# Performance work log

Measured on AMD Instinct MI355X. Metric: run time of the kernel, lower is better.

Reference implementation:

```python
import jax, jax.numpy as jnp
import numpy as np
import math

DMODEL = 1024
N_EXPERTS = 32
EXPERT_SIZE = 512
N_HEADS = 4
TOKENS = 4096


def setup_inputs() -> dict:
    key = jax.random.key(0)
    k1, k2, k3, k4 = jax.random.split(key, 4)
    x = jax.random.normal(k1, (TOKENS, DMODEL), dtype=jnp.float32)
    keys_w = jax.random.normal(k2, (N_EXPERTS, DMODEL, EXPERT_SIZE), dtype=jnp.float32) * (DMODEL ** -0.5)
    values_w = jax.random.normal(k3, (N_EXPERTS, EXPERT_SIZE, DMODEL), dtype=jnp.float32) * ((N_EXPERTS * EXPERT_SIZE) ** -0.5)
    es = jax.random.normal(k4, (N_EXPERTS, DMODEL), dtype=jnp.float32) * (DMODEL ** -0.5)
    # renorm_keep_std(expert_sel, dim=1): row-normalize, then rescale to original global std
    std0 = jnp.std(es)
    es_n = es / jnp.linalg.norm(es, axis=1, keepdims=True)
    expert_sel = es_n * (std0 / jnp.std(es_n))
    return {"x": x, "keys": keys_w, "values": values_w, "expert_sel": expert_sel, "n_heads": N_HEADS}


def reference(x, keys, values, expert_sel, n_heads):
    # x: [T, d]; keys: [E, d, h]; values: [E, h, d]; expert_sel: [E, d]
    T, d = x.shape
    E = keys.shape[0]

    # routing logits
    sel_raw = x @ expert_sel.T  # [T, E]

    # entropy regularizer: mean (in log space) over tokens of log-softmax, then negative entropy
    logp = jax.nn.log_softmax(sel_raw, axis=-1)                 # [T, E]
    lm = jax.scipy.special.logsumexp(logp, axis=0) - math.log(T)  # [E]
    reg_loss = jnp.sum(lm * jnp.exp(lm))                        # -entropy_l(lm)

    # sigmoid selection + top-k experts per token
    sel = jax.nn.sigmoid(sel_raw)
    sel_val, sel_idx = jax.lax.top_k(sel, n_heads)              # [T, H]

    # expert up-projection (grouped GEMM): compute dense then gather selected experts
    scores_all = jnp.einsum('td,edh->teh', x, keys)             # [T, E, h]
    scores = jnp.take_along_axis(scores_all, sel_idx[:, :, None], axis=1)  # [T, H, h]
    scores = jax.nn.relu(scores) * sel_val[..., None]

    # combine: scatter weighted scores back to expert slots, then down-project
    onehot = jax.nn.one_hot(sel_idx, E, dtype=x.dtype)          # [T, H, E]
    dispatched = jnp.einsum('the,ths->tes', onehot, scores)     # [T, E, h]
    out = jnp.einsum('tes,esd->td', dispatched, values)         # [T, d]
    return out, reg_loss
```

## Files before the change

kernel.cpp:

```cpp
#include <hip/hip_runtime.h>
#include <hip/hip_bf16.h>

typedef unsigned short u16;
typedef unsigned int u32;
typedef __attribute__((ext_vector_type(4))) float f32x4;
typedef __attribute__((ext_vector_type(8))) short bf16x8;

#define TOKENS 4096
#define DMODEL 1024
#define NEXP 32
#define ESIZE 512

__device__ __forceinline__ u16 f2b(float f) {
  union { float f; u32 u; } v; v.f = f;
  u32 u = v.u;
  return (u16)((u + 0x7fffu + ((u >> 16) & 1u)) >> 16);
}

__device__ __forceinline__ u32 pk2(float a, float b) {
  union { __hip_bfloat162 h; u32 u; } v;
  v.h = __float22bfloat162_rn(make_float2(a, b));
  return v.u;
}

__device__ __forceinline__ float blo(u32 w) { union { u32 u; float f; } v; v.u = w << 16; return v.f; }
__device__ __forceinline__ float bhi(u32 w) { union { u32 u; float f; } v; v.u = w & 0xffff0000u; return v.f; }

typedef __attribute__((address_space(1))) const void as1_void;
typedef __attribute__((address_space(3))) void as3_void;
__device__ __forceinline__ void gl16(const void* g, void* l) {
  __builtin_amdgcn_global_load_lds((as1_void*)g, (as3_void*)l, 16, 0, 0);
}

__device__ __forceinline__ int swz(int row, int kk) {
  return row * 72 + ((((kk >> 3) ^ (row >> 2)) & 7) << 3) + (kk & 7);
}

__global__ __launch_bounds__(256) void k_esT(const float* __restrict__ es,
                                             float* __restrict__ esT4)
{
  int tid = threadIdx.x;
  int dblk = (blockIdx.x << 3) + (tid >> 5);
  int e = tid & 31;
  float4 v = *(const float4*)(es + (size_t)e * DMODEL + (dblk << 2));
  *((float4*)esT4 + (size_t)dblk * 32 + e) = v;
}

__device__ __forceinline__ void tr_tile(const float* __restrict__ src,
                                        u16* __restrict__ dst, int R, int C,
                                        int cx, int cy, int e, int t, float* smemf)
{
  float (*tile)[68] = (float(*)[68])smemf;
  int r0 = cy << 6, c0 = cx << 6;
  int rr = t >> 2, cb = (t & 3) << 4;
  const float* sp = src + ((size_t)e * R + r0 + rr) * C + c0 + cb;
#pragma unroll
  for (int j = 0; j < 4; ++j)
    *(float4*)&tile[rr][cb + (j << 2)] = *(const float4*)(sp + (j << 2));
  __syncthreads();
  int wr = t >> 2, wb = (t & 3) << 4;
  u32 q[8];
#pragma unroll
  for (int j = 0; j < 8; ++j)
    q[j] = pk2(tile[wb + (j << 1)][wr], tile[wb + (j << 1) + 1][wr]);
  u16* dp = dst + ((size_t)e * C + c0 + wr) * R + r0 + wb;
  *(uint4*)dp = make_uint4(q[0], q[1], q[2], q[3]);
  *(uint4*)(dp + 8) = make_uint4(q[4], q[5], q[6], q[7]);
}

__global__ __launch_bounds__(256) void k_mega1(
    const float* __restrict__ x, const float* __restrict__ esT4,
    float* __restrict__ selval, u32* __restrict__ selpk,
    float* __restrict__ blockpart, u16* __restrict__ xb,
    const float* __restrict__ keys, const float* __restrict__ values,
    u16* __restrict__ kb, u16* __restrict__ vb)
{
  __shared__ __align__(16) float smem[4352];
  int bid = blockIdx.x;
  int tid = threadIdx.x;

  if (bid >= 512 + 4096) {
    int i = bid - (512 + 4096);
    tr_tile(values, vb, ESIZE, DMODEL, i & 15, (i >> 4) & 7, i >> 7, tid, smem);
    return;
  }
  if (bid >= 512) {
    int i = bid - 512;
    tr_tile(keys, kb, DMODEL, ESIZE, i & 7, (i >> 3) & 15, i >> 7, tid, smem);
    return;
  }

  float (*part)[8][32] = (float(*)[8][32])smem;
  float (*ps)[32] = (float(*)[32])(smem + 1024);
  int w = tid >> 6, lane = tid & 63;
  int e = lane & 31, h = lane >> 5;
  int t0 = bid << 3;

  const float4* ev = (const float4*)esT4 + (size_t)((w << 6) + (h << 5)) * 32 + e;
  const float4* xv = (const float4*)x + ((size_t)t0 << 8) + (w << 6) + (h << 5);

  float acc[8];
#pragma unroll
  for (int tk = 0; tk < 8; ++tk) acc[tk] = 0.f;

#pragma unroll 2
  for (int i = 0; i < 32; ++i) {
    float4 b = ev[(size_t)i * 32];
#pragma unroll
    for (int tk = 0; tk < 8; ++tk) {
      float4 a = xv[(tk << 8) + i];
      acc[tk] += a.x * b.x + a.y * b.y + a.z * b.z + a.w * b.w;
    }
  }
#pragma unroll
  for (int tk = 0; tk < 8; ++tk) {
    float s = acc[tk] + __shfl_xor(acc[tk], 32);
    if (h == 0) part[w][tk][e] = s;
  }
  __syncthreads();

  int tk = tid >> 5, ge = tid & 31;
  {
    float r = part[0][tk][ge] + part[1][tk][ge] + part[2][tk][ge] + part[3][tk][ge];
    int t = t0 + tk;

    float m = r;
#pragma unroll
    for (int mk = 16; mk; mk >>= 1) m = fmaxf(m, __shfl_xor(m, mk));
    float sx = __expf(r - m);
#pragma unroll
    for (int mk = 16; mk; mk >>= 1) sx += __shfl_xor(sx, mk);
    ps[tk][ge] = __expf(r - (m + __logf(sx)));

    u32 packed = 0;
    float v = r;
#pragma unroll
    for (int it = 0; it < 4; ++it) {
      float bv = v; int bi = ge;
#pragma unroll
      for (int mk = 16; mk; mk >>= 1) {
        float ov = __shfl_xor(bv, mk); int oi = __shfl_xor(bi, mk);
        if (ov > bv || (ov == bv && oi < bi)) { bv = ov; bi = oi; }
      }
      packed |= (u32)bi << (8 * it);
      if (ge == it) selval[t * 4 + it] = 1.f / (1.f + __expf(-bv));
      if (ge == bi) v = -3.0e38f;
    }
    if (ge == 0) selpk[t] = packed;
  }
  __syncthreads();
  if (tid < 32) {
    float s = 0.f;
#pragma unroll
    for (int j = 0; j < 8; ++j) s += ps[j][tid];
    blockpart[bid * 32 + tid] = s;
  }

  if (xb) {
    const float4* src = (const float4*)x + ((size_t)bid << 11);
    u16* dst = xb + ((size_t)bid << 13);
#pragma unroll
    for (int j = 0; j < 8; ++j) {
      int idx = (j << 8) + tid;
      float4 a = src[idx];
      *(uint2*)(dst + (idx << 2)) = make_uint2(pk2(a.x, a.y), pk2(a.z, a.w));
    }
  }
}

__global__ __launch_bounds__(1024) void k_count(
    const u32* __restrict__ selpk, int* __restrict__ cnt, int* __restrict__ bucket)
{
  __shared__ int cl[32];
  int tid = threadIdx.x;
  if (tid < 32) cl[tid] = 0;
  __syncthreads();
  int ex[16], pos[16];
#pragma unroll
  for (int j = 0; j < 4; ++j) {
    int t = tid + (j << 10);
    u32 pk = selpk[t];
#pragma unroll
    for (int h = 0; h < 4; ++h) {
      int e = (pk >> (8 * h)) & 0xff;
      ex[j * 4 + h] = e;
      pos[j * 4 + h] = atomicAdd(&cl[e], 1);
    }
  }
#pragma unroll
  for (int j = 0; j < 4; ++j) {
    int t = tid + (j << 10);
#pragma unroll
    for (int h = 0; h < 4; ++h)
      bucket[ex[j * 4 + h] * TOKENS + pos[j * 4 + h]] = (t << 2) | h;
  }
  __syncthreads();
  if (tid < 32) cnt[tid] = cl[tid];
}

__global__ __launch_bounds__(256) void k_fin(const float* __restrict__ blockpart,
                                             float* __restrict__ out_reg)
{
  __shared__ float part[8][32];
  int tid = threadIdx.x;
  int e = tid & 31, c = tid >> 5;
  float s = 0.f;
  for (int b = c; b < 512; b += 8) s += blockpart[b * 32 + e];
  part[c][e] = s;
  __syncthreads();
  if (tid < 32) {
    float S = 0.f;
#pragma unroll
    for (int i = 0; i < 8; ++i) S += part[i][tid];
    float Pm = S * (1.0f / TOKENS);
    float rp = __logf(Pm) * Pm;
#pragma unroll
    for (int mk = 16; mk; mk >>= 1) rp += __shfl_xor(rp, mk);
    if (tid == 0) *out_reg = rp;
  }
}

#define GEMM_MACROS                                                                          \
  int wm = (w >> 1) << 6, wn = (w & 1) << 6;                                                 \
  int w32 = w << 5;                                                                          \
  int lg16 = (((l & 7) ^ (l >> 3)) << 4);

#define STAGE(BUF, K0) do {                                                                  \
  _Pragma("unroll") for (int i_ = 0; i_ < 4; ++i_)                                           \
    gl16(gA[i_] + ((K0) << 1), (void*)&Ab[BUF][(((w << 2) + i_) << 9)]);                     \
  _Pragma("unroll") for (int i_ = 0; i_ < 4; ++i_)                                           \
    gl16(gB[i_] + ((K0) << 1), (void*)&Bb[BUF][(((w << 2) + i_) << 9)]);                     \
} while (0)

#define COMPUTE(CUR) do {                                                                    \
  _Pragma("unroll") for (int kh_ = 0; kh_ < 2; ++kh_) {                                      \
    bf16x8 af_[4], bf_[4];                                                                   \
    int gg_ = (kh_ << 2) + (l >> 4);                                                         \
    _Pragma("unroll") for (int mi_ = 0; mi_ < 4; ++mi_) {                                    \
      int row_ = wm + (mi_ << 4) + (l & 15);                                                 \
      af_[mi_] = *(const bf16x8*)&Ab[CUR][(row_ << 6) + ((gg_ ^ (row_ & 7)) << 3)];          \
    }                                                                                        \
    _Pragma("unroll") for (int ni_ = 0; ni_ < 4; ++ni_) {                                    \
      int row_ = wn + (ni_ << 4) + (l & 15);                                                 \
      bf_[ni_] = *(const bf16x8*)&Bb[CUR][(row_ << 6) + ((gg_ ^ (row_ & 7)) << 3)];          \
    }                                                                                        \
    _Pragma("unroll") for (int mi_ = 0; mi_ < 4; ++mi_)                                      \
      _Pragma("unroll") for (int ni_ = 0; ni_ < 4; ++ni_)                                    \
        acc[mi_][ni_] = __builtin_amdgcn_mfma_f32_16x16x32_bf16(af_[mi_], bf_[ni_],          \
                                                                acc[mi_][ni_], 0, 0, 0);     \
  }                                                                                          \
} while (0)

#define KLOOP(NT) do {                                                                       \
  STAGE(0, 0);                                                                               \
  STAGE(1, 64);                                                                              \
  _Pragma("unroll 1")                                                                        \
  for (int t_ = 0; t_ < (NT); ++t_) {                                                        \
    int cur_ = t_ & 1;                                                                       \
    if (t_ + 1 < (NT)) { asm volatile("s_waitcnt vmcnt(8)" ::: "memory"); }                  \
    else               { asm volatile("s_waitcnt vmcnt(0)" ::: "memory"); }                  \
    asm volatile("s_barrier" ::: "memory");                                                  \
    COMPUTE(cur_);                                                                           \
    asm volatile("s_barrier" ::: "memory");                                                  \
    if (t_ + 2 < (NT)) STAGE(cur_, (t_ + 2) << 6);                                           \
  }                                                                                          \
} while (0)

#define XCD_DECODE(SUB_NS_BITS)                                                              \
  int bid = blockIdx.x;                                                                      \
  int q_ = bid >> 3, sub_ = q_ & 15;                                                         \
  int e = ((q_ >> 4) << 3) | (bid & 7);                                                      \
  int ns = sub_ & ((1 << (SUB_NS_BITS)) - 1);                                                \
  int mz = sub_ >> (SUB_NS_BITS);

__global__ __launch_bounds__(256, 2) void k_up(
    const u16* __restrict__ xb, const u16* __restrict__ kb,
    const float* __restrict__ selval, const int* __restrict__ cnt,
    const int* __restrict__ bucket, const u16* __restrict__ zeros,
    u16* __restrict__ scores)
{
  XCD_DECODE(2);
  int ne = cnt[e];
  if ((mz << 7) >= ne) return;
  int nb0 = ns << 7;
  int tid = threadIdx.x, l = tid & 63, w = tid >> 6;

  __shared__ __align__(16) u16 Ab[2][8192];
  __shared__ __align__(16) u16 Bb[2][8192];
  __shared__ int slot_l[128];
  __shared__ float gate_l[128];

  GEMM_MACROS;

  const char* gB[4];
#pragma unroll
  for (int i = 0; i < 4; ++i) {
    int n = nb0 + w32 + (i << 3) + (l >> 3);
    gB[i] = (const char*)(kb + ((size_t)e * ESIZE + n) * DMODEL) + lg16;
  }

  for (int mt = mz; (mt << 7) < ne; mt += 4) {
    int row0 = mt << 7;
    int rem = ne - row0; if (rem > 128) rem = 128;
    __syncthreads();
    if (tid < 128) {
      int slot = -1; float g = 0.f;
      if (tid < rem) { slot = bucket[e * TOKENS + row0 + tid]; g = selval[slot]; }
      slot_l[tid] = slot; gate_l[tid] = g;
    }
    __syncthreads();

    const char* gA[4];
#pragma unroll
    for (int i = 0; i < 4; ++i) {
      int s = slot_l[w32 + (i << 3) + (l >> 3)];
      gA[i] = ((s >= 0) ? (const char*)(xb + (size_t)(s >> 2) * DMODEL)
                        : (const char*)zeros) + lg16;
    }

    f32x4 acc[4][4];
#pragma unroll
    for (int i = 0; i < 4; ++i)
#pragma unroll
      for (int j = 0; j < 4; ++j) acc[i][j] = (f32x4){0.f, 0.f, 0.f, 0.f};

    KLOOP(16);

#pragma unroll
    for (int mi = 0; mi < 4; ++mi) {
      int rbase = wm + (mi << 4) + ((l >> 4) << 2);
#pragma unroll
      for (int rr = 0; rr < 4; ++rr) {
        int r = rbase + rr;
        if (r < rem) {
          float g = gate_l[r];
          u16* so = scores + (size_t)slot_l[r] * ESIZE + nb0 + wn + (l & 15);
#pragma unroll
          for (int ni = 0; ni < 4; ++ni)
            so[ni << 4] = f2b(fmaxf(acc[mi][ni][rr], 0.f) * g);
        }
      }
    }
  }
}

__global__ __launch_bounds__(256, 2) void k_down(
    const u16* __restrict__ scores, const u16* __restrict__ vb,
    const int* __restrict__ cnt, const int* __restrict__ bucket,
    const u16* __restrict__ zeros, u16* __restrict__ stage)
{
  XCD_DECODE(3);
  int ne = cnt[e];
  if ((mz << 7) >= ne) return;
  int nb0 = ns << 7;
  int tid = threadIdx.x, l = tid & 63, w = tid >> 6;

  __shared__ __align__(16) u16 Ab[2][8192];
  __shared__ __align__(16) u16 Bb[2][8192];
  __shared__ int slot_l[128];

  GEMM_MACROS;

  const char* gB[4];
#pragma unroll
  for (int i = 0; i < 4; ++i) {
    int n = nb0 + w32 + (i << 3) + (l >> 3);
    gB[i] = (const char*)(vb + ((size_t)e * DMODEL + n) * ESIZE) + lg16;
  }

  for (int mt = mz; (mt << 7) < ne; mt += 2) {
    int row0 = mt << 7;
    int rem = ne - row0; if (rem > 128) rem = 128;
    __syncthreads();
    if (tid < 128) {
      int slot = -1;
      if (tid < rem) slot = bucket[e * TOKENS + row0 + tid];
      slot_l[tid] = slot;
    }
    __syncthreads();

    const char* gA[4];
#pragma unroll
    for (int i = 0; i < 4; ++i) {
      int s = slot_l[w32 + (i << 3) + (l >> 3)];
      gA[i] = ((s >= 0) ? (const char*)(scores + (size_t)s * ESIZE)
                        : (const char*)zeros) + lg16;
    }

    f32x4 acc[4][4];
#pragma unroll
    for (int i = 0; i < 4; ++i)
#pragma unroll
      for (int j = 0; j < 4; ++j) acc[i][j] = (f32x4){0.f, 0.f, 0.f, 0.f};

    KLOOP(8);

#pragma unroll
    for (int mi = 0; mi < 4; ++mi) {
      int rbase = wm + (mi << 4) + ((l >> 4) << 2);
#pragma unroll
      for (int rr = 0; rr < 4; ++rr) {
        int r = rbase + rr;
        if (r < rem) {
          u16* so = stage + (size_t)slot_l[r] * DMODEL + nb0 + wn + (l & 15);
#pragma unroll
          for (int ni = 0; ni < 4; ++ni)
            so[ni << 4] = f2b(acc[mi][ni][rr]);
        }
      }
    }
  }
}

__global__ __launch_bounds__(256) void k_final(const u16* __restrict__ stage,
                                               float* __restrict__ out)
{
  int tid = threadIdx.x;
  int t = (blockIdx.x << 1) + (tid >> 7);
  int d0 = (tid & 127) << 3;
  const u16* r0 = stage + ((size_t)t << 12) + d0;
  uint4 a0 = *(const uint4*)(r0);
  uint4 a1 = *(const uint4*)(r0 + 1024);
  uint4 a2 = *(const uint4*)(r0 + 2048);
  uint4 a3 = *(const uint4*)(r0 + 3072);
  float4 lo4, hi4;
  lo4.x = blo(a0.x) + blo(a1.x) + blo(a2.x) + blo(a3.x);
  lo4.y = bhi(a0.x) + bhi(a1.x) + bhi(a2.x) + bhi(a3.x);
  lo4.z = blo(a0.y) + blo(a1.y) + blo(a2.y) + blo(a3.y);
  lo4.w = bhi(a0.y) + bhi(a1.y) + bhi(a2.y) + bhi(a3.y);
  hi4.x = blo(a0.z) + blo(a1.z) + blo(a2.z) + blo(a3.z);
  hi4.y = bhi(a0.z) + bhi(a1.z) + bhi(a2.z) + bhi(a3.z);
  hi4.z = blo(a0.w) + blo(a1.w) + blo(a2.w) + blo(a3.w);
  hi4.w = bhi(a0.w) + bhi(a1.w) + bhi(a2.w) + bhi(a3.w);
  float* o = out + (size_t)t * DMODEL + d0;
  *(float4*)o = lo4;
  *(float4*)(o + 4) = hi4;
}

__global__ __launch_bounds__(256, 2) void k_up_rs(
    const float* __restrict__ x, const float* __restrict__ keys,
    const float* __restrict__ selval, const int* __restrict__ cnt,
    const int* __restrict__ bucket, u16* __restrict__ scores)
{
  int bid = blockIdx.x;
  int pair = bid & 127, mz = bid >> 7;
  int e = pair >> 2, ns = pair & 3;
  int ne = cnt[e];
  if ((mz << 7) >= ne) return;
  int nb0 = ns << 7;
  int tid = threadIdx.x;

  __shared__ __align__(16) u16 Abuf[2][128 * 72];
  __shared__ __align__(16) u16 Bbuf[2][128 * 72];
  __shared__ int slot_l[128];
  __shared__ float gate_l[128];

  const float* Kb = keys + (size_t)e * (DMODEL * ESIZE) + nb0;
  int arow = tid >> 1, ac0 = (tid & 1) << 5;
  int bn = tid & 31, bk0 = (tid >> 5) << 3;
  int lane = tid & 63, w = tid >> 6;
  int wm = (w >> 1) << 6, wn = (w & 1) << 6;

  for (int mt = mz; (mt << 7) < ne; mt += 4) {
    int row0 = mt << 7;
    int rem = ne - row0; if (rem > 128) rem = 128;
    __syncthreads();
    if (tid < 128) {
      int slot = -1; float g = 0.f;
      if (tid < rem) { slot = bucket[e * TOKENS + row0 + tid]; g = selval[slot]; }
      slot_l[tid] = slot; gate_l[tid] = g;
    }
    __syncthreads();

    int aslot = slot_l[arow];
    const float* xr = (aslot >= 0) ? (x + (size_t)(aslot >> 2) * DMODEL + ac0) : nullptr;
    const float* bp = Kb + (size_t)bk0 * ESIZE + (bn << 2);

    f32x4 acc[4][4];
#pragma unroll
    for (int i = 0; i < 4; ++i)
#pragma unroll
      for (int j = 0; j < 4; ++j) acc[i][j] = (f32x4){0.f, 0.f, 0.f, 0.f};

    float4 ar[8], br[8];
#define LOADA_UP(K) do { if (xr) { const float4* p_ = (const float4*)(xr + (K)); \
    _Pragma("unroll") for (int i_ = 0; i_ < 8; ++i_) ar[i_] = p_[i_]; } \
    else { _Pragma("unroll") for (int i_ = 0; i_ < 8; ++i_) ar[i_] = make_float4(0.f,0.f,0.f,0.f); } } while (0)
#define LOADB_RS(K, LDB) do { const float* q_ = bp + (size_t)(K) * (LDB); \
    _Pragma("unroll") for (int r_ = 0; r_ < 8; ++r_) br[r_] = *(const float4*)(q_ + (size_t)r_ * (LDB)); } while (0)
#define CVTWR_A(NB) do { _Pragma("unroll") for (int g_ = 0; g_ < 4; ++g_) { \
    u32 q0_ = pk2(ar[2*g_].x, ar[2*g_].y),   q1_ = pk2(ar[2*g_].z, ar[2*g_].w); \
    u32 q2_ = pk2(ar[2*g_+1].x, ar[2*g_+1].y), q3_ = pk2(ar[2*g_+1].z, ar[2*g_+1].w); \
    *(uint4*)&Abuf[NB][swz(arow, ac0 + 8*g_)] = make_uint4(q0_,q1_,q2_,q3_); } } while (0)
#define CVTWR_B(NB) do { \
    { u32 q0_=pk2(br[0].x,br[1].x),q1_=pk2(br[2].x,br[3].x),q2_=pk2(br[4].x,br[5].x),q3_=pk2(br[6].x,br[7].x); \
      *(uint4*)&Bbuf[NB][swz((bn<<2)+0, bk0)] = make_uint4(q0_,q1_,q2_,q3_); } \
    { u32 q0_=pk2(br[0].y,br[1].y),q1_=pk2(br[2].y,br[3].y),q2_=pk2(br[4].y,br[5].y),q3_=pk2(br[6].y,br[7].y); \
      *(uint4*)&Bbuf[NB][swz((bn<<2)+1, bk0)] = make_uint4(q0_,q1_,q2_,q3_); } \
    { u32 q0_=pk2(br[0].z,br[1].z),q1_=pk2(br[2].z,br[3].z),q2_=pk2(br[4].z,br[5].z),q3_=pk2(br[6].z,br[7].z); \
      *(uint4*)&Bbuf[NB][swz((bn<<2)+2, bk0)] = make_uint4(q0_,q1_,q2_,q3_); } \
    { u32 q0_=pk2(br[0].w,br[1].w),q1_=pk2(br[2].w,br[3].w),q2_=pk2(br[4].w,br[5].w),q3_=pk2(br[6].w,br[7].w); \
      *(uint4*)&Bbuf[NB][swz((bn<<2)+3, bk0)] = make_uint4(q0_,q1_,q2_,q3_); } } while (0)
#define MFMA_RS(CUR) do { _Pragma("unroll") for (int kh_ = 0; kh_ < 2; ++kh_) { \
    int kk_ = (kh_ << 5) | ((lane >> 4) << 3); \
    bf16x8 af_[4], bf_[4]; \
    _Pragma("unroll") for (int mi_ = 0; mi_ < 4; ++mi_) \
      af_[mi_] = *(const bf16x8*)&Abuf[CUR][swz(wm + (mi_ << 4) + (lane & 15), kk_)]; \
    _Pragma("unroll") for (int ni_ = 0; ni_ < 4; ++ni_) \
      bf_[ni_] = *(const bf16x8*)&Bbuf[CUR][swz(wn + (ni_ << 4) + (lane & 15), kk_)]; \
    _Pragma("unroll") for (int mi_ = 0; mi_ < 4; ++mi_) \
      _Pragma("unroll") for (int ni_ = 0; ni_ < 4; ++ni_) \
        acc[mi_][ni_] = __builtin_amdgcn_mfma_f32_16x16x32_bf16(af_[mi_], bf_[ni_], acc[mi_][ni_], 0, 0, 0); \
  } } while (0)

    LOADA_UP(0); LOADB_RS(0, ESIZE);
    CVTWR_A(0); CVTWR_B(0);
    __syncthreads();
    int cur = 0;
    for (int k0 = 0; k0 < DMODEL; k0 += 64) {
      bool late = (k0 + 64 >= DMODEL);
      if (!late) { LOADA_UP(k0 + 64); LOADB_RS(k0 + 64, ESIZE); }
      MFMA_RS(cur);
      if (!late) { CVTWR_A(cur ^ 1); CVTWR_B(cur ^ 1); }
      __syncthreads();
      cur ^= 1;
    }

#pragma unroll
    for (int mi = 0; mi < 4; ++mi) {
      int rbase = wm + (mi << 4) + ((lane >> 4) << 2);
#pragma unroll
      for (int rr = 0; rr < 4; ++rr) {
        int r = rbase + rr;
        if (r < rem) {
          float g = gate_l[r];
          u16* so = scores + (size_t)slot_l[r] * ESIZE + nb0 + wn + (lane & 15);
#pragma unroll
          for (int ni = 0; ni < 4; ++ni)
            so[ni << 4] = f2b(fmaxf(acc[mi][ni][rr], 0.f) * g);
        }
      }
    }
#undef LOADA_UP
#undef LOADB_RS
#undef CVTWR_A
#undef CVTWR_B
#undef MFMA_RS
  }
}

__global__ __launch_bounds__(256, 2) void k_down_rs(
    const u16* __restrict__ scores, const float* __restrict__ values,
    const int* __restrict__ cnt, const int* __restrict__ bucket,
    u16* __restrict__ stage, float* __restrict__ out)
{
  int bid = blockIdx.x;
  int pair = bid & 255, mz = bid >> 8;
  int e = pair >> 3, ns = pair & 7;
  int ne = cnt[e];
  if ((mz << 7) >= ne) return;
  int nb0 = ns << 7;
  int tid = threadIdx.x;

  __shared__ __align__(16) u16 Abuf[2][128 * 72];
  __shared__ __align__(16) u16 Bbuf[2][128 * 72];
  __shared__ int slot_l[128];

  const float* Vb = values + (size_t)e * (ESIZE * DMODEL) + nb0;
  int arow = tid >> 1, ac0 = (tid & 1) << 5;
  int bn = tid & 31, bk0 = (tid >> 5) << 3;
  int lane = tid & 63, w = tid >> 6;
  int wm = (w >> 1) << 6, wn = (w & 1) << 6;

  for (int mt = mz; (mt << 7) < ne; mt += 2) {
    int row0 = mt << 7;
    int rem = ne - row0; if (rem > 128) rem = 128;
    __syncthreads();
    if (tid < 128) {
      int slot = -1;
      if (tid < rem) slot = bucket[e * TOKENS + row0 + tid];
      slot_l[tid] = slot;
    }
    __syncthreads();

    int aslot = slot_l[arow];
    const u16* sr = (aslot >= 0) ? (scores + (size_t)aslot * ESIZE + ac0) : nullptr;
    const float* bp = Vb + (size_t)bk0 * DMODEL + (bn << 2);

    f32x4 acc[4][4];
#pragma unroll
    for (int i = 0; i < 4; ++i)
#pragma unroll
      for (int j = 0; j < 4; ++j) acc[i][j] = (f32x4){0.f, 0.f, 0.f, 0.f};

    uint4 a4[4]; float4 br[8];
#define LOADA_DN(K) do { if (sr) { const uint4* p_ = (const uint4*)(sr + (K)); \
    _Pragma("unroll") for (int i_ = 0; i_ < 4; ++i_) a4[i_] = p_[i_]; } \
    else { _Pragma("unroll") for (int i_ = 0; i_ < 4; ++i_) a4[i_] = make_uint4(0,0,0,0); } } while (0)
#define LOADB_RS(K, LDB) do { const float* q_ = bp + (size_t)(K) * (LDB); \
    _Pragma("unroll") for (int r_ = 0; r_ < 8; ++r_) br[r_] = *(const float4*)(q_ + (size_t)r_ * (LDB)); } while (0)
#define WR_A(NB) do { _Pragma("unroll") for (int g_ = 0; g_ < 4; ++g_) \
    *(uint4*)&Abuf[NB][swz(arow, ac0 + 8*g_)] = a4[g_]; } while (0)
#define CVTWR_B(NB) do { \
    { u32 q0_=pk2(br[0].x,br[1].x),q1_=pk2(br[2].x,br[3].x),q2_=pk2(br[4].x,br[5].x),q3_=pk2(br[6].x,br[7].x); \
      *(uint4*)&Bbuf[NB][swz((bn<<2)+0, bk0)] = make_uint4(q0_,q1_,q2_,q3_); } \
    { u32 q0_=pk2(br[0].y,br[1].y),q1_=pk2(br[2].y,br[3].y),q2_=pk2(br[4].y,br[5].y),q3_=pk2(br[6].y,br[7].y); \
      *(uint4*)&Bbuf[NB][swz((bn<<2)+1, bk0)] = make_uint4(q0_,q1_,q2_,q3_); } \
    { u32 q0_=pk2(br[0].z,br[1].z),q1_=pk2(br[2].z,br[3].z),q2_=pk2(br[4].z,br[5].z),q3_=pk2(br[6].z,br[7].z); \
      *(uint4*)&Bbuf[NB][swz((bn<<2)+2, bk0)] = make_uint4(q0_,q1_,q2_,q3_); } \
    { u32 q0_=pk2(br[0].w,br[1].w),q1_=pk2(br[2].w,br[3].w),q2_=pk2(br[4].w,br[5].w),q3_=pk2(br[6].w,br[7].w); \
      *(uint4*)&Bbuf[NB][swz((bn<<2)+3, bk0)] = make_uint4(q0_,q1_,q2_,q3_); } } while (0)
#define MFMA_RS(CUR) do { _Pragma("unroll") for (int kh_ = 0; kh_ < 2; ++kh_) { \
    int kk_ = (kh_ << 5) | ((lane >> 4) << 3); \
    bf16x8 af_[4], bf_[4]; \
    _Pragma("unroll") for (int mi_ = 0; mi_ < 4; ++mi_) \
      af_[mi_] = *(const bf16x8*)&Abuf[CUR][swz(wm + (mi_ << 4) + (lane & 15), kk_)]; \
    _Pragma("unroll") for (int ni_ = 0; ni_ < 4; ++ni_) \
      bf_[ni_] = *(const bf16x8*)&Bbuf[CUR][swz(wn + (ni_ << 4) + (lane & 15), kk_)]; \
    _Pragma("unroll") for (int mi_ = 0; mi_ < 4; ++mi_) \
      _Pragma("unroll") for (int ni_ = 0; ni_ < 4; ++ni_) \
        acc[mi_][ni_] = __builtin_amdgcn_mfma_f32_16x16x32_bf16(af_[mi_], bf_[ni_], acc[mi_][ni_], 0, 0, 0); \
  } } while (0)

    LOADA_DN(0); LOADB_RS(0, DMODEL);
    WR_A(0); CVTWR_B(0);
    __syncthreads();
    int cur = 0;
    for (int k0 = 0; k0 < ESIZE; k0 += 64) {
      bool late = (k0 + 64 >= ESIZE);
      if (!late) { LOADA_DN(k0 + 64); LOADB_RS(k0 + 64, DMODEL); }
      MFMA_RS(cur);
      if (!late) { WR_A(cur ^ 1); CVTWR_B(cur ^ 1); }
      __syncthreads();
      cur ^= 1;
    }

#pragma unroll
    for (int mi = 0; mi < 4; ++mi) {
      int rbase = wm + (mi << 4) + ((lane >> 4) << 2);
#pragma unroll
      for (int rr = 0; rr < 4; ++rr) {
        int r = rbase + rr;
        if (r < rem) {
          if (stage) {
            u16* so = stage + (size_t)slot_l[r] * DMODEL + nb0 + wn + (lane & 15);
#pragma unroll
            for (int ni = 0; ni < 4; ++ni)
              so[ni << 4] = f2b(acc[mi][ni][rr]);
          } else {
            int t = slot_l[r] >> 2;
            float* oo = out + (size_t)t * DMODEL + nb0 + wn + (lane & 15);
#pragma unroll
            for (int ni = 0; ni < 4; ++ni)
              atomicAdd(&oo[ni << 4], acc[mi][ni][rr]);
          }
        }
      }
    }
#undef LOADA_DN
#undef LOADB_RS
#undef WR_A
#undef CVTWR_B
#undef MFMA_RS
  }
}

extern "C" void kernel_launch(void* const* d_in, const int* in_sizes, int n_in,
                              void* d_out, int out_size, void* d_ws, size_t ws_size,
                              hipStream_t stream) {
  (void)in_sizes; (void)n_in;
  const float* x      = (const float*)d_in[0];
  const float* keys   = (const float*)d_in[1];
  const float* values = (const float*)d_in[2];
  const float* es     = (const float*)d_in[3];
  float* out = (float*)d_out;

  char* W = (char*)d_ws;
  int*   cnt       = (int*)W;
  u16*   zeros     = (u16*)(W + 4 * 1024);
  u32*   selpk     = (u32*)(W + 16 * 1024);
  float* selval    = (float*)(W + 64 * 1024);
  float* blockpart = (float*)(W + 128 * 1024);
  int*   bucket    = (int*)(W + 512 * 1024);
  float* esT4      = (float*)(W + 1280 * 1024);

  bool big = ws_size >= (90ull << 20);

  k_esT<<<32, 256, 0, stream>>>(es, esT4);

  if (big) {
    u16* xb     = (u16*)(W + 2ull * 1024 * 1024);
    u16* scores = (u16*)(W + 10ull * 1024 * 1024);
    u16* kb     = (u16*)(W + 26ull * 1024 * 1024);
    u16* vb     = (u16*)(W + 58ull * 1024 * 1024);
    u16* stage  = kb;
    hipMemsetAsync(zeros, 0, 4096, stream);
    k_mega1<<<512 + 4096 + 4096, 256, 0, stream>>>(
        x, esT4, selval, selpk, blockpart, xb, keys, values, kb, vb);
    k_count<<<1, 1024, 0, stream>>>(selpk, cnt, bucket);
    k_fin<<<1, 256, 0, stream>>>(blockpart, out + (size_t)out_size - 1);
    k_up<<<512, 256, 0, stream>>>(xb, kb, selval, cnt, bucket, zeros, scores);
    k_down<<<512, 256, 0, stream>>>(scores, vb, cnt, bucket, zeros, stage);
    k_final<<<TOKENS / 2, 256, 0, stream>>>(stage, out);
  } else {
    u16* scores = (u16*)(W + 2ull * 1024 * 1024);
    bool big50 = ws_size >= (50ull << 20);
    u16* stage = big50 ? (u16*)(W + 18ull * 1024 * 1024) : nullptr;
    if (!big50)
      hipMemsetAsync(d_out, 0, (size_t)out_size * sizeof(float), stream);
    k_mega1<<<512, 256, 0, stream>>>(
        x, esT4, selval, selpk, blockpart, nullptr, nullptr, nullptr, nullptr, nullptr);
    k_count<<<1, 1024, 0, stream>>>(selpk, cnt, bucket);
    k_fin<<<1, 256, 0, stream>>>(blockpart, out + (size_t)out_size - 1);
    k_up_rs<<<512, 256, 0, stream>>>(x, keys, selval, cnt, bucket, scores);
    k_down_rs<<<512, 256, 0, stream>>>(scores, values, cnt, bucket, stage, out);
    if (big50)
      k_final<<<TOKENS / 2, 256, 0, stream>>>(stage, out);
  }
}
```

Baseline: 159.2 us.

## Halve GEMM K-tile to raise occupancy and fuse count with regularizer finalize

The grouped up/down GEMM kernels now stage K=32 slices instead of K=64. This halves the LDS footprint, and the swizzle and load pointers are rebuilt for 32-element rows. Launch bounds rise to 4 blocks per CU, so more waves can hide memory latency, at the cost of twice as many barrier-separated iterations with less MFMA work each. The single-block count kernel and the regularizer finalize kernel are merged into one launch to drop one kernel launch.

After: 165.7 us. +4.0%, slower.

```diff
diff --git a/kernel.cpp b/kernel.cpp
--- a/kernel.cpp
+++ b/kernel.cpp
@@ -168,10 +168,12 @@
   }
 }
 
-__global__ __launch_bounds__(1024) void k_count(
-    const u32* __restrict__ selpk, int* __restrict__ cnt, int* __restrict__ bucket)
+__global__ __launch_bounds__(1024) void k_cf(
+    const u32* __restrict__ selpk, int* __restrict__ cnt, int* __restrict__ bucket,
+    const float* __restrict__ blockpart, float* __restrict__ out_reg)
 {
   __shared__ int cl[32];
+  __shared__ float pf[32][33];
   int tid = threadIdx.x;
   if (tid < 32) cl[tid] = 0;
   __syncthreads();
@@ -196,22 +198,16 @@
   }
   __syncthreads();
   if (tid < 32) cnt[tid] = cl[tid];
-}
-
-__global__ __launch_bounds__(256) void k_fin(const float* __restrict__ blockpart,
-                                             float* __restrict__ out_reg)
-{
-  __shared__ float part[8][32];
-  int tid = threadIdx.x;
+
   int e = tid & 31, c = tid >> 5;
   float s = 0.f;
-  for (int b = c; b < 512; b += 8) s += blockpart[b * 32 + e];
-  part[c][e] = s;
+  for (int b = c; b < 512; b += 32) s += blockpart[b * 32 + e];
+  pf[c][e] = s;
   __syncthreads();
   if (tid < 32) {
     float S = 0.f;
 #pragma unroll
-    for (int i = 0; i < 8; ++i) S += part[i][tid];
+    for (int i = 0; i < 32; ++i) S += pf[i][tid];
     float Pm = S * (1.0f / TOKENS);
     float rp = __logf(Pm) * Pm;
 #pragma unroll
@@ -222,47 +218,45 @@
 
 #define GEMM_MACROS                                                                          \
   int wm = (w >> 1) << 6, wn = (w & 1) << 6;                                                 \
-  int w32 = w << 5;                                                                          \
-  int lg16 = (((l & 7) ^ (l >> 3)) << 4);
+  int lsub = l >> 2;                                                                         \
+  int lg16 = (((l & 3) ^ (lsub & 3)) << 4);
 
 #define STAGE(BUF, K0) do {                                                                  \
-  _Pragma("unroll") for (int i_ = 0; i_ < 4; ++i_)                                           \
-    gl16(gA[i_] + ((K0) << 1), (void*)&Ab[BUF][(((w << 2) + i_) << 9)]);                     \
-  _Pragma("unroll") for (int i_ = 0; i_ < 4; ++i_)                                           \
-    gl16(gB[i_] + ((K0) << 1), (void*)&Bb[BUF][(((w << 2) + i_) << 9)]);                     \
+  gl16(gA0 + ((K0) << 1), (void*)&Ab[BUF][(w << 10)]);                                       \
+  gl16(gA1 + ((K0) << 1), (void*)&Ab[BUF][(w << 10) + 512]);                                 \
+  gl16(gB0 + ((K0) << 1), (void*)&Bb[BUF][(w << 10)]);                                       \
+  gl16(gB1 + ((K0) << 1), (void*)&Bb[BUF][(w << 10) + 512]);                                 \
 } while (0)
 
 #define COMPUTE(CUR) do {                                                                    \
-  _Pragma("unroll") for (int kh_ = 0; kh_ < 2; ++kh_) {                                      \
-    bf16x8 af_[4], bf_[4];                                                                   \
-    int gg_ = (kh_ << 2) + (l >> 4);                                                         \
-    _Pragma("unroll") for (int mi_ = 0; mi_ < 4; ++mi_) {                                    \
-      int row_ = wm + (mi_ << 4) + (l & 15);                                                 \
-      af_[mi_] = *(const bf16x8*)&Ab[CUR][(row_ << 6) + ((gg_ ^ (row_ & 7)) << 3)];          \
-    }                                                                                        \
-    _Pragma("unroll") for (int ni_ = 0; ni_ < 4; ++ni_) {                                    \
-      int row_ = wn + (ni_ << 4) + (l & 15);                                                 \
-      bf_[ni_] = *(const bf16x8*)&Bb[CUR][(row_ << 6) + ((gg_ ^ (row_ & 7)) << 3)];          \
-    }                                                                                        \
-    _Pragma("unroll") for (int mi_ = 0; mi_ < 4; ++mi_)                                      \
-      _Pragma("unroll") for (int ni_ = 0; ni_ < 4; ++ni_)                                    \
-        acc[mi_][ni_] = __builtin_amdgcn_mfma_f32_16x16x32_bf16(af_[mi_], bf_[ni_],          \
-                                                                acc[mi_][ni_], 0, 0, 0);     \
+  bf16x8 af_[4], bf_[4];                                                                     \
+  int gg_ = l >> 4;                                                                          \
+  _Pragma("unroll") for (int mi_ = 0; mi_ < 4; ++mi_) {                                      \
+    int row_ = wm + (mi_ << 4) + (l & 15);                                                   \
+    af_[mi_] = *(const bf16x8*)&Ab[CUR][(row_ << 5) + ((gg_ ^ (row_ & 3)) << 3)];            \
   }                                                                                          \
+  _Pragma("unroll") for (int ni_ = 0; ni_ < 4; ++ni_) {                                      \
+    int row_ = wn + (ni_ << 4) + (l & 15);                                                   \
+    bf_[ni_] = *(const bf16x8*)&Bb[CUR][(row_ << 5) + ((gg_ ^ (row_ & 3)) << 3)];            \
+  }                                                                                          \
+  _Pragma("unroll") for (int mi_ = 0; mi_ < 4; ++mi_)                                        \
+    _Pragma("unroll") for (int ni_ = 0; ni_ < 4; ++ni_)                                      \
+      acc[mi_][ni_] = __builtin_amdgcn_mfma_f32_16x16x32_bf16(af_[mi_], bf_[ni_],            \
+                                                              acc[mi_][ni_], 0, 0, 0);       \
 } while (0)
 
 #define KLOOP(NT) do {                                                                       \
   STAGE(0, 0);                                                                               \
-  STAGE(1, 64);                                                                              \
+  STAGE(1, 32);                                                                              \
   _Pragma("unroll 1")                                                                        \
   for (int t_ = 0; t_ < (NT); ++t_) {                                                        \
     int cur_ = t_ & 1;                                                                       \
-    if (t_ + 1 < (NT)) { asm volatile("s_waitcnt vmcnt(8)" ::: "memory"); }                  \
+    if (t_ + 1 < (NT)) { asm volatile("s_waitcnt vmcnt(4)" ::: "memory"); }                  \
     else               { asm volatile("s_waitcnt vmcnt(0)" ::: "memory"); }                  \
     asm volatile("s_barrier" ::: "memory");                                                  \
     COMPUTE(cur_);                                                                           \
     asm volatile("s_barrier" ::: "memory");                                                  \
-    if (t_ + 2 < (NT)) STAGE(cur_, (t_ + 2) << 6);                                           \
+    if (t_ + 2 < (NT)) STAGE(cur_, (t_ + 2) << 5);                                           \
   }                                                                                          \
 } while (0)
 
@@ -273,7 +267,7 @@
   int ns = sub_ & ((1 << (SUB_NS_BITS)) - 1);                                                \
   int mz = sub_ >> (SUB_NS_BITS);
 
-__global__ __launch_bounds__(256, 2) void k_up(
+__global__ __launch_bounds__(256, 4) void k_up(
     const u16* __restrict__ xb, const u16* __restrict__ kb,
     const float* __restrict__ selval, const int* __restrict__ cnt,
     const int* __restrict__ bucket, const u16* __restrict__ zeros,
@@ -285,19 +279,16 @@
   int nb0 = ns << 7;
   int tid = threadIdx.x, l = tid & 63, w = tid >> 6;
 
-  __shared__ __align__(16) u16 Ab[2][8192];
-  __shared__ __align__(16) u16 Bb[2][8192];
+  __shared__ __align__(16) u16 Ab[2][4096];
+  __shared__ __align__(16) u16 Bb[2][4096];
   __shared__ int slot_l[128];
   __shared__ float gate_l[128];
 
   GEMM_MACROS;
 
-  const char* gB[4];
-#pragma unroll
-  for (int i = 0; i < 4; ++i) {
-    int n = nb0 + w32 + (i << 3) + (l >> 3);
-    gB[i] = (const char*)(kb + ((size_t)e * ESIZE + n) * DMODEL) + lg16;
-  }
+  int ra0 = (w << 5) + lsub, ra1 = ra0 + 16;
+  const char* gB0 = (const char*)(kb + ((size_t)e * ESIZE + nb0 + ra0) * DMODEL) + lg16;
+  const char* gB1 = gB0 + (size_t)16 * DMODEL * sizeof(u16);
 
   for (int mt = mz; (mt << 7) < ne; mt += 4) {
     int row0 = mt << 7;
@@ -310,13 +301,11 @@
     }
     __syncthreads();
 
-    const char* gA[4];
-#pragma unroll
-    for (int i = 0; i < 4; ++i) {
-      int s = slot_l[w32 + (i << 3) + (l >> 3)];
-      gA[i] = ((s >= 0) ? (const char*)(xb + (size_t)(s >> 2) * DMODEL)
-                        : (const char*)zeros) + lg16;
-    }
+    int s0 = slot_l[ra0], s1 = slot_l[ra1];
+    const char* gA0 = ((s0 >= 0) ? (const char*)(xb + (size_t)(s0 >> 2) * DMODEL)
+                                 : (const char*)zeros) + lg16;
+    const char* gA1 = ((s1 >= 0) ? (const char*)(xb + (size_t)(s1 >> 2) * DMODEL)
+                                 : (const char*)zeros) + lg16;
 
     f32x4 acc[4][4];
 #pragma unroll
@@ -324,7 +313,7 @@
 #pragma unroll
       for (int j = 0; j < 4; ++j) acc[i][j] = (f32x4){0.f, 0.f, 0.f, 0.f};
 
-    KLOOP(16);
+    KLOOP(32);
 
 #pragma unroll
     for (int mi = 0; mi < 4; ++mi) {
@@ -344,7 +333,7 @@
   }
 }
 
-__global__ __launch_bounds__(256, 2) void k_down(
+__global__ __launch_bounds__(256, 4) void k_down(
     const u16* __restrict__ scores, const u16* __restrict__ vb,
     const int* __restrict__ cnt, const int* __restrict__ bucket,
     const u16* __restrict__ zeros, u16* __restrict__ stage)
@@ -355,18 +344,15 @@
   int nb0 = ns << 7;
   int tid = threadIdx.x, l = tid & 63, w = tid >> 6;
 
-  __shared__ __align__(16) u16 Ab[2][8192];
-  __shared__ __align__(16) u16 Bb[2][8192];
+  __shared__ __align__(16) u16 Ab[2][4096];
+  __shared__ __align__(16) u16 Bb[2][4096];
   __shared__ int slot_l[128];
 
   GEMM_MACROS;
 
-  const char* gB[4];
-#pragma unroll
-  for (int i = 0; i < 4; ++i) {
-    int n = nb0 + w32 + (i << 3) + (l >> 3);
-    gB[i] = (const char*)(vb + ((size_t)e * DMODEL + n) * ESIZE) + lg16;
-  }
+  int ra0 = (w << 5) + lsub, ra1 = ra0 + 16;
+  const char* gB0 = (const char*)(vb + ((size_t)e * DMODEL + nb0 + ra0) * ESIZE) + lg16;
+  const char* gB1 = gB0 + (size_t)16 * ESIZE * sizeof(u16);
 
   for (int mt = mz; (mt << 7) < ne; mt += 2) {
     int row0 = mt << 7;
@@ -379,13 +365,11 @@
     }
     __syncthreads();
 
-    const char* gA[4];
-#pragma unroll
-    for (int i = 0; i < 4; ++i) {
-      int s = slot_l[w32 + (i << 3) + (l >> 3)];
-      gA[i] = ((s >= 0) ? (const char*)(scores + (size_t)s * ESIZE)
-                        : (const char*)zeros) + lg16;
-    }
+    int s0 = slot_l[ra0], s1 = slot_l[ra1];
+    const char* gA0 = ((s0 >= 0) ? (const char*)(scores + (size_t)s0 * ESIZE)
+                                 : (const char*)zeros) + lg16;
+    const char* gA1 = ((s1 >= 0) ? (const char*)(scores + (size_t)s1 * ESIZE)
+                                 : (const char*)zeros) + lg16;
 
     f32x4 acc[4][4];
 #pragma unroll
@@ -393,7 +377,7 @@
 #pragma unroll
       for (int j = 0; j < 4; ++j) acc[i][j] = (f32x4){0.f, 0.f, 0.f, 0.f};
 
-    KLOOP(8);
+    KLOOP(16);
 
 #pragma unroll
     for (int mi = 0; mi < 4; ++mi) {
@@ -697,8 +681,8 @@
     hipMemsetAsync(zeros, 0, 4096, stream);
     k_mega1<<<512 + 4096 + 4096, 256, 0, stream>>>(
         x, esT4, selval, selpk, blockpart, xb, keys, values, kb, vb);
-    k_count<<<1, 1024, 0, stream>>>(selpk, cnt, bucket);
-    k_fin<<<1, 256, 0, stream>>>(blockpart, out + (size_t)out_size - 1);
+    k_cf<<<1, 1024, 0, stream>>>(selpk, cnt, bucket, blockpart,
+                                 out + (size_t)out_size - 1);
     k_up<<<512, 256, 0, stream>>>(xb, kb, selval, cnt, bucket, zeros, scores);
     k_down<<<512, 256, 0, stream>>>(scores, vb, cnt, bucket, zeros, stage);
     k_final<<<TOKENS / 2, 256, 0, stream>>>(stage, out);
@@ -710,8 +694,8 @@
       hipMemsetAsync(d_out, 0, (size_t)out_size * sizeof(float), stream);
     k_mega1<<<512, 256, 0, stream>>>(
         x, esT4, selval, selpk, blockpart, nullptr, nullptr, nullptr, nullptr, nullptr);
-    k_count<<<1, 1024, 0, stream>>>(selpk, cnt, bucket);
-    k_fin<<<1, 256, 0, stream>>>(blockpart, out + (size_t)out_size - 1);
+    k_cf<<<1, 1024, 0, stream>>>(selpk, cnt, bucket, blockpart,
+                                 out + (size_t)out_size - 1);
     k_up_rs<<<512, 256, 0, stream>>>(x, keys, selval, cnt, bucket, scores);
     k_down_rs<<<512, 256, 0, stream>>>(scores, values, cnt, bucket, stage, out);
     if (big50)
```
